# Performance work log

Measured on AMD Instinct MI355X. Metric: run time of the kernel, lower is better.

The kernel has to match this reference:

```python
import jax, jax.numpy as jnp
import numpy as np

DIM = 64
B = 4
NQ = 4096
NK = 4096
N_ENTRIES = 4


def setup_inputs() -> dict:
    key = jax.random.key(0)
    kq, kk, kc, kp = jax.random.split(key, 4)
    return {
        "queries": jax.random.normal(kq, (B, NQ, DIM), dtype=jnp.float32),
        "keys": jax.random.normal(kk, (B, NK, DIM), dtype=jnp.float32),
        "center": jax.random.normal(kc, (DIM,), dtype=jnp.float32) * 0.1,
        "outer_radius": jnp.asarray(1.0, dtype=jnp.float32),
        # 0.2 is within the module's clamp range [0.01, 0.4] (post gentle_evolution)
        # and exercises the full torus-surface branch (hole_ratio >= 0.1).
        "hole_radius": jnp.asarray(0.2, dtype=jnp.float32),
        "entry_points": jax.random.normal(kp, (N_ENTRIES, DIM), dtype=jnp.float32) * 0.2,
        "entry_strengths": jnp.zeros((N_ENTRIES,), dtype=jnp.float32),
        "amplitude": jnp.asarray(1.0, dtype=jnp.float32),
    }


def _torus_surface_distance(point_dists, outer_radius, hole_radius):
    outer_r = jnp.abs(outer_radius) + 1e-8
    hole_r = jnp.abs(hole_radius)
    hole_ratio = hole_r / outer_r
    major = jnp.abs(point_dists - outer_r)
    torus = jnp.abs(jnp.sqrt(major * major + hole_r * hole_r) - hole_r)
    return jnp.where(hole_ratio < 0.1, major, torus)


def reference(queries, keys, center, outer_radius, hole_radius,
              entry_points, entry_strengths, amplitude):
    # distances of queries/keys to the splat center: [B, N]
    q_dists = jnp.linalg.norm(queries - center, axis=-1)
    k_dists = jnp.linalg.norm(keys - center, axis=-1)
    q_surf = _torus_surface_distance(q_dists, outer_radius, hole_radius)  # [B, Nq]
    k_surf = _torus_surface_distance(k_dists, outer_radius, hole_radius)  # [B, Nk]
    # exp(-0.5 (q^2 + k^2)) factorizes into an outer product of per-side exps
    surface_attention = jnp.exp(-0.5 * (q_surf[:, :, None] ** 2 + k_surf[:, None, :] ** 2))  # [B,Nq,Nk]

    # entry-point rank-1 terms; active mask (sigmoid(strength) > 0.1) folded into weight
    strengths = jax.nn.sigmoid(entry_strengths)                 # [E]
    w = jnp.where(strengths > 0.1, strengths, 0.0)              # [E]
    # cdist(queries, entry_points): [B, Nq, E]
    q_ed = jnp.linalg.norm(queries[:, :, None, :] - entry_points[None, None, :, :], axis=-1)
    k_ed = jnp.linalg.norm(keys[:, :, None, :] - entry_points[None, None, :, :], axis=-1)
    q_entry = jnp.exp(-0.5 * q_ed * q_ed)                       # [B, Nq, E]
    k_entry = jnp.exp(-0.5 * k_ed * k_ed)                       # [B, Nk, E]
    entry_attention = jnp.einsum("bqe,bke,e->bqk", q_entry, k_entry, w)

    return amplitude * (surface_attention + entry_attention)
```

## Files before the change

### kernel.cpp

```cpp
#include <hip/hip_runtime.h>
#include <math.h>

#define DIM 64
#define NE 4
#define B_SZ 4
#define NQ 4096
#define NK 4096
#define BQ 8

typedef float fvec4 __attribute__((ext_vector_type(4)));

__global__ __launch_bounds__(256) void feat_kernel(
    const float* __restrict__ queries,
    const float* __restrict__ keys,
    const float* __restrict__ center,
    const float* __restrict__ outer_radius,
    const float* __restrict__ hole_radius,
    const float* __restrict__ entry_points,
    const float* __restrict__ entry_strengths,
    const float* __restrict__ amplitude,
    float* __restrict__ qf,
    float* __restrict__ kf)
{
    const int row = blockIdx.x * blockDim.x + threadIdx.x;
    const int nqrows = B_SZ * NQ;
    const bool is_q = row < nqrows;
    const int  r    = is_q ? row : row - nqrows;
    const float* src = (is_q ? queries : keys) + (size_t)r * DIM;

    float a0 = 0.f, a1 = 0.f, a2 = 0.f, a3 = 0.f, a4 = 0.f;

    #pragma unroll
    for (int j = 0; j < DIM / 4; ++j) {
        const fvec4 v  = *reinterpret_cast<const fvec4*>(src + j * 4);
        const fvec4 c  = *reinterpret_cast<const fvec4*>(center + j * 4);
        const fvec4 p0 = *reinterpret_cast<const fvec4*>(entry_points + 0 * DIM + j * 4);
        const fvec4 p1 = *reinterpret_cast<const fvec4*>(entry_points + 1 * DIM + j * 4);
        const fvec4 p2 = *reinterpret_cast<const fvec4*>(entry_points + 2 * DIM + j * 4);
        const fvec4 p3 = *reinterpret_cast<const fvec4*>(entry_points + 3 * DIM + j * 4);
        #pragma unroll
        for (int cc = 0; cc < 4; ++cc) {
            const float x  = v[cc];
            const float d0 = x - c[cc];
            const float d1 = x - p0[cc];
            const float d2 = x - p1[cc];
            const float d3 = x - p2[cc];
            const float d4 = x - p3[cc];
            a0 += d0 * d0;
            a1 += d1 * d1;
            a2 += d2 * d2;
            a3 += d3 * d3;
            a4 += d4 * d4;
        }
    }

    const float outer_r    = fabsf(outer_radius[0]) + 1e-8f;
    const float hole_r     = fabsf(hole_radius[0]);
    const float hole_ratio = hole_r / outer_r;
    const float amp        = amplitude[0];

    const float dist  = sqrtf(a0);
    const float major = fabsf(dist - outer_r);
    const float torus = fabsf(sqrtf(major * major + hole_r * hole_r) - hole_r);
    const float surf  = (hole_ratio < 0.1f) ? major : torus;

    const float f0 = expf(-0.5f * surf * surf);
    const float f1 = expf(-0.5f * a1);
    const float f2 = expf(-0.5f * a2);
    const float f3 = expf(-0.5f * a3);
    const float f4 = expf(-0.5f * a4);

    const int b = r >> 12;
    const int n = r & (NQ - 1);

    if (is_q) {
        float* dst = qf + ((size_t)b * 5) * NQ + n;
        dst[0 * NQ] = amp * f0;
        dst[1 * NQ] = amp * f1;
        dst[2 * NQ] = amp * f2;
        dst[3 * NQ] = amp * f3;
        dst[4 * NQ] = amp * f4;
    } else {
        float w[NE];
        #pragma unroll
        for (int e = 0; e < NE; ++e) {
            float s = 1.0f / (1.0f + expf(-entry_strengths[e]));
            w[e] = (s > 0.1f) ? s : 0.0f;
        }
        float* dst = kf + ((size_t)b * 5) * NK + n;
        dst[0 * NK] = f0;
        dst[1 * NK] = w[0] * f1;
        dst[2 * NK] = w[1] * f2;
        dst[3 * NK] = w[2] * f3;
        dst[4 * NK] = w[3] * f4;
    }
}

__global__ __launch_bounds__(256) void write_kernel(
    const float* __restrict__ qf,
    const float* __restrict__ kf,
    float* __restrict__ out)
{
    const int b   = blockIdx.y;
    const int q0  = blockIdx.x * BQ;
    const int tid = threadIdx.x;

    const float* qfb = qf + ((size_t)b * 5) * NQ + q0;
    const float* kfb = kf + ((size_t)b * 5) * NK;

    float qv[5][BQ];
    #pragma unroll
    for (int e = 0; e < 5; ++e) {
        fvec4 lo = *reinterpret_cast<const fvec4*>(qfb + (size_t)e * NQ);
        fvec4 hi = *reinterpret_cast<const fvec4*>(qfb + (size_t)e * NQ + 4);
        qv[e][0] = lo.x; qv[e][1] = lo.y; qv[e][2] = lo.z; qv[e][3] = lo.w;
        qv[e][4] = hi.x; qv[e][5] = hi.y; qv[e][6] = hi.z; qv[e][7] = hi.w;
    }

    float* ob = out + ((size_t)(b * NQ + q0)) * NK;

    #pragma unroll
    for (int cg = 0; cg < NK / 1024; ++cg) {
        const int k0 = cg * 1024 + tid * 4;
        fvec4 kc[5];
        #pragma unroll
        for (int e = 0; e < 5; ++e)
            kc[e] = *reinterpret_cast<const fvec4*>(kfb + (size_t)e * NK + k0);

        #pragma unroll
        for (int r = 0; r < BQ; ++r) {
            fvec4 v = qv[0][r] * kc[0] + qv[1][r] * kc[1] + qv[2][r] * kc[2]
                    + qv[3][r] * kc[3] + qv[4][r] * kc[4];
            __builtin_nontemporal_store(v, reinterpret_cast<fvec4*>(ob + (size_t)r * NK + k0));
        }
    }
}

extern "C" void kernel_launch(void* const* d_in, const int* in_sizes, int n_in,
                              void* d_out, int out_size, void* d_ws, size_t ws_size,
                              hipStream_t stream) {
    const float* queries         = (const float*)d_in[0];
    const float* keys            = (const float*)d_in[1];
    const float* center          = (const float*)d_in[2];
    const float* outer_radius    = (const float*)d_in[3];
    const float* hole_radius     = (const float*)d_in[4];
    const float* entry_points    = (const float*)d_in[5];
    const float* entry_strengths = (const float*)d_in[6];
    const float* amplitude       = (const float*)d_in[7];

    float* qf = (float*)d_ws;
    float* kf = qf + (size_t)B_SZ * 5 * NQ;
    float* out = (float*)d_out;

    {
        const int total_rows = B_SZ * NQ + B_SZ * NK;
        feat_kernel<<<total_rows / 256, 256, 0, stream>>>(
            queries, keys, center, outer_radius, hole_radius,
            entry_points, entry_strengths, amplitude, qf, kf);
    }

    {
        dim3 grid(NQ / BQ, B_SZ);
        write_kernel<<<grid, 256, 0, stream>>>(qf, kf, out);
    }
}
```

Before: 59.83 us.

## Use persistent grid-stride chunks for output write kernel

Replaces the per-block 8-row tiling with a fixed grid of 2048 blocks that each stride over 1024-element output chunks, so consecutive blocks write consecutive memory. Each chunk reloads its query features and key feature vectors instead of reusing them across 8 rows. It also switches the nontemporal vector stores to regular stores. The aim is smoother streaming of the large output write, at the cost of extra feature loads and the loss of the cache-bypass hint.

Measured after the change: 69.75 us. +16.6%, slower.

```diff
diff --git a/kernel.cpp b/kernel.cpp
--- a/kernel.cpp
+++ b/kernel.cpp
@@ -6,7 +6,9 @@
 #define B_SZ 4
 #define NQ 4096
 #define NK 4096
-#define BQ 8
+
+#define WG 2048
+#define TOTAL_CHUNKS (B_SZ * NQ * 4)
 
 typedef float fvec4 __attribute__((ext_vector_type(4)));
 
@@ -101,38 +103,32 @@
     const float* __restrict__ kf,
     float* __restrict__ out)
 {
-    const int b   = blockIdx.y;
-    const int q0  = blockIdx.x * BQ;
     const int tid = threadIdx.x;
 
-    const float* qfb = qf + ((size_t)b * 5) * NQ + q0;
-    const float* kfb = kf + ((size_t)b * 5) * NK;
+    #pragma unroll 2
+    for (int i = 0; i < TOTAL_CHUNKS / WG; ++i) {
+        const int chunk = blockIdx.x + i * WG;
+        const int cg = chunk & 3;
+        const int q  = (chunk >> 2) & (NQ - 1);
+        const int b  = chunk >> 14;
 
-    float qv[5][BQ];
-    #pragma unroll
-    for (int e = 0; e < 5; ++e) {
-        fvec4 lo = *reinterpret_cast<const fvec4*>(qfb + (size_t)e * NQ);
-        fvec4 hi = *reinterpret_cast<const fvec4*>(qfb + (size_t)e * NQ + 4);
-        qv[e][0] = lo.x; qv[e][1] = lo.y; qv[e][2] = lo.z; qv[e][3] = lo.w;
-        qv[e][4] = hi.x; qv[e][5] = hi.y; qv[e][6] = hi.z; qv[e][7] = hi.w;
-    }
+        const float* qfb = qf + ((size_t)b * 5) * NQ + q;
+        const float q0 = qfb[0 * NQ];
+        const float q1 = qfb[1 * NQ];
+        const float q2 = qfb[2 * NQ];
+        const float q3 = qfb[3 * NQ];
+        const float q4 = qfb[4 * NQ];
 
-    float* ob = out + ((size_t)(b * NQ + q0)) * NK;
+        const int k0 = cg * 1024 + tid * 4;
+        const float* kfb = kf + ((size_t)b * 5) * NK + k0;
 
-    #pragma unroll
-    for (int cg = 0; cg < NK / 1024; ++cg) {
-        const int k0 = cg * 1024 + tid * 4;
-        fvec4 kc[5];
-        #pragma unroll
-        for (int e = 0; e < 5; ++e)
-            kc[e] = *reinterpret_cast<const fvec4*>(kfb + (size_t)e * NK + k0);
+        fvec4 v = q0 * *reinterpret_cast<const fvec4*>(kfb + 0 * (size_t)NK)
+                + q1 * *reinterpret_cast<const fvec4*>(kfb + 1 * (size_t)NK)
+                + q2 * *reinterpret_cast<const fvec4*>(kfb + 2 * (size_t)NK)
+                + q3 * *reinterpret_cast<const fvec4*>(kfb + 3 * (size_t)NK)
+                + q4 * *reinterpret_cast<const fvec4*>(kfb + 4 * (size_t)NK);
 
-        #pragma unroll
-        for (int r = 0; r < BQ; ++r) {
-            fvec4 v = qv[0][r] * kc[0] + qv[1][r] * kc[1] + qv[2][r] * kc[2]
-                    + qv[3][r] * kc[3] + qv[4][r] * kc[4];
-            __builtin_nontemporal_store(v, reinterpret_cast<fvec4*>(ob + (size_t)r * NK + k0));
-        }
+        *reinterpret_cast<fvec4*>(out + ((size_t)chunk << 10) + tid * 4) = v;
     }
 }
 
@@ -160,7 +156,6 @@
     }
 
     {
-        dim3 grid(NQ / BQ, B_SZ);
-        write_kernel<<<grid, 256, 0, stream>>>(qf, kf, out);
+        write_kernel<<<WG, 256, 0, stream>>>(qf, kf, out);
     }
 }
```
